# Optimization experiments

Hardware: AMD Instinct MI355X
Metric: run time of the kernel (lower is better)

## Reference

```python
import jax, jax.numpy as jnp
import numpy as np

L = 256  # grayscale_levels
THRESH = (50.0, 150.0)
BASE = (30, 80, 150)
INCR = (10, 15, 25)


def setup_inputs() -> dict:
    key = jax.random.key(0)
    image = jax.random.uniform(key, (8, 3, 1024, 1024), dtype=jnp.float32)
    return {"image": image}


def _glcm_contrast(gray_idx):
    # gray_idx: [H, W] int32 in [0, L). distance=1, angle=0 -> horizontal neighbor pairs.
    p1 = gray_idx[:, :-1].ravel()
    p2 = gray_idx[:, 1:].ravel()
    # 256x256 co-occurrence histogram via flattened scatter-add
    hist = jnp.zeros(L * L, jnp.float32).at[p1 * L + p2].add(1.0)
    hist = hist / jnp.float32(p1.size)
    lv = jnp.arange(L, dtype=jnp.float32)
    diff2 = (lv[:, None] - lv[None, :]) ** 2
    return jnp.sum(hist.reshape(L, L) * diff2)


def _grid_labels(H, W, n_segments):
    # Deterministic grid superpixels (stand-in for skimage SLIC's initial grid;
    # same downstream math: fill each segment with its region mean).
    gr = max(1, int(round(np.sqrt(n_segments * H / W))))
    gc = max(1, int(np.ceil(n_segments / gr)))
    r = (np.arange(H) * gr) // H
    c = (np.arange(W) * gc) // W
    labels = r[:, None] * gc + c[None, :]
    return jnp.asarray(labels, dtype=jnp.int32), gr * gc


def _region_mean_saliency(gray, labels, nseg):
    flat = labels.ravel()
    sums = jax.ops.segment_sum(gray.ravel(), flat, num_segments=nseg)
    cnts = jax.ops.segment_sum(jnp.ones_like(gray).ravel(), flat, num_segments=nseg)
    return (sums / jnp.maximum(cnts, 1.0))[labels]


def reference(image):
    B, C, H, W = image.shape
    gray = 0.299 * image[:, 0] + 0.587 * image[:, 1] + 0.114 * image[:, 2]
    gidx = jnp.clip((gray * (L - 1)).astype(jnp.int32), 0, L - 1)
    complexity = jax.vmap(_glcm_contrast)(gidx)  # [B]

    comp_np = np.asarray(jax.device_get(complexity))
    cluster_sets = []
    for cv in comp_np:
        tier = 0 if cv < THRESH[0] else (1 if cv < THRESH[1] else 2)
        k, d = BASE[tier], INCR[tier]
        cluster_sets.append([k - d, k, k + d])

    # region mean uses np.mean over all channels of the region -> channel-mean image
    chan_mean = image.mean(axis=1)  # [B, H, W]
    label_cache = {}
    sal_rows = []
    for i, cset in enumerate(cluster_sets):
        maps = []
        for n in cset:
            if n not in label_cache:
                label_cache[n] = _grid_labels(H, W, n)
            labels, nseg = label_cache[n]
            maps.append(_region_mean_saliency(chan_mean[i], labels, nseg))
        sal_rows.append(jnp.stack(maps))  # [3, H, W]
    saliency = jnp.stack(sal_rows)  # [B, 3, H, W]
    return saliency, complexity, jnp.asarray(cluster_sets, dtype=jnp.int32)
```

## Files before the change

### kernel.cpp

```cpp
#include <hip/hip_runtime.h>
#include <math.h>

#define HW 1024
#define PLANE (1024 * 1024)

typedef float vf4 __attribute__((ext_vector_type(4)));

__constant__ int GCS[8]   = {5, 6, 7, 9, 10, 12, 13, 14};
__constant__ int BBASE[8] = {0, 6, 13, 21, 31, 42, 55, 69};
__constant__ int GR9c[9]      = {4, 5, 6, 8, 9, 10, 11, 12, 13};
__constant__ int GC9c[9]      = {5, 6, 7, 9, 9, 10, 12, 13, 14};
__constant__ int COLBASE9c[9] = {0, 5, 11, 18, 18, 27, 37, 49, 62};


__device__ __forceinline__ int wave_reduce_int(int v) {
#pragma unroll
    for (int off = 32; off > 0; off >>= 1) v += __shfl_down(v, off, 64);
    return v;
}
__device__ __forceinline__ float wave_reduce_f(float v) {
#pragma unroll
    for (int off = 32; off > 0; off >>= 1) v += __shfl_down(v, off, 64);
    return v;
}

__device__ __forceinline__ unsigned short f2bf(float x) {
    unsigned int u = __float_as_uint(x);
    u += 0x7fff + ((u >> 16) & 1);
    return (unsigned short)(u >> 16);
}
__device__ __forceinline__ float bf2f(unsigned short s) {
    return __uint_as_float(((unsigned int)s) << 16);
}

__global__ __launch_bounds__(256) void k_main(const float* __restrict__ img,
                                              float* __restrict__ partials,
                                              float* __restrict__ rowrec) {
    const int b = blockIdx.y;
    const int tid = threadIdx.x;
    const int lane = tid & 63;
    const int w = tid >> 6;
    const int row = (blockIdx.x << 2) + w;

    const float* p = img + (size_t)b * (3 * PLANE) + row * HW;

    __shared__ unsigned short cmS[4][1024];
    __shared__ float PS[4][260];
    __shared__ float BS[4][88];
    __shared__ int swred[4];

    vf4 R[4], G[4], Bv[4];
#pragma unroll
    for (int j = 0; j < 4; ++j) {
        const int c = ((j << 6) + lane) << 2;
        R[j] = __builtin_nontemporal_load((const vf4*)(p + c));
        G[j] = __builtin_nontemporal_load((const vf4*)(p + PLANE + c));
        Bv[j] = __builtin_nontemporal_load((const vf4*)(p + 2 * PLANE + c));
    }

    int acc = 0;
    int pend = 0;
    float csum[4];

#pragma unroll
    for (int j = 0; j < 4; ++j) {
        const int c = ((j << 6) + lane) << 2;

        const float m0 = (R[j].x + G[j].x + Bv[j].x) * (1.0f / 3.0f);
        const float m1 = (R[j].y + G[j].y + Bv[j].y) * (1.0f / 3.0f);
        const float m2 = (R[j].z + G[j].z + Bv[j].z) * (1.0f / 3.0f);
        const float m3 = (R[j].w + G[j].w + Bv[j].w) * (1.0f / 3.0f);
        *(ushort4*)&cmS[w][c] = make_ushort4(f2bf(m0), f2bf(m1), f2bf(m2), f2bf(m3));
        csum[j] = (m0 + m1) + (m2 + m3);

        const float g0 = 0.299f * R[j].x + 0.587f * G[j].x + 0.114f * Bv[j].x;
        const float g1 = 0.299f * R[j].y + 0.587f * G[j].y + 0.114f * Bv[j].y;
        const float g2 = 0.299f * R[j].z + 0.587f * G[j].z + 0.114f * Bv[j].z;
        const float g3 = 0.299f * R[j].w + 0.587f * G[j].w + 0.114f * Bv[j].w;

        const int gi0 = min(max((int)(g0 * 255.0f), 0), 255);
        const int gi1 = min(max((int)(g1 * 255.0f), 0), 255);
        const int gi2 = min(max((int)(g2 * 255.0f), 0), 255);
        const int gi3 = min(max((int)(g3 * 255.0f), 0), 255);

        const int first0 = __shfl(gi0, 0, 64);
        if (j > 0 && lane == 63) {
            const int d = pend - first0;
            acc += d * d;
        }
        const int nxt = __shfl_down(gi0, 1, 64);
        const int d0 = gi0 - gi1, d1 = gi1 - gi2, d2 = gi2 - gi3;
        acc += d0 * d0 + d1 * d1 + d2 * d2;
        if (lane != 63) {
            const int d = gi3 - nxt;
            acc += d * d;
        }
        pend = gi3;
    }

    float pre = 0.0f;
#pragma unroll
    for (int j = 0; j < 4; ++j) {
        float x = csum[j];
#pragma unroll
        for (int off = 1; off < 64; off <<= 1) {
            const float y = __shfl_up(x, off, 64);
            if (lane >= off) x += y;
        }
        PS[w][(j << 6) + lane] = pre + (x - csum[j]);
        pre += __shfl(x, 63, 64);
    }
    if (lane == 0) PS[w][256] = pre;

#pragma unroll
    for (int rep = 0; rep < 2; ++rep) {
        const int bnd = lane + (rep << 6);
        if (bnd < 84) {
            const int sct = (bnd >= 6) + (bnd >= 13) + (bnd >= 21) + (bnd >= 31) +
                            (bnd >= 42) + (bnd >= 55) + (bnd >= 69);
            const int gc = GCS[sct];
            const int i = bnd - BBASE[sct];
            const int c = (i * 1024 + gc - 1) / gc;
            const int m = c & 3;
            const int cb = min(c & ~3, 1020);
            float Bp = PS[w][c >> 2];
            const float a0 = bf2f(cmS[w][cb]), a1 = bf2f(cmS[w][cb + 1]),
                        a2 = bf2f(cmS[w][cb + 2]);
            if (m > 0) Bp += a0;
            if (m > 1) Bp += a1;
            if (m > 2) Bp += a2;
            BS[w][bnd] = Bp;
        }
    }

    float* rr = rowrec + (size_t)((b << 10) + row) * 80;
#pragma unroll
    for (int rep = 0; rep < 2; ++rep) {
        const int k = lane + (rep << 6);
        if (k < 76) {
            const int sct = (k >= 5) + (k >= 11) + (k >= 18) + (k >= 27) +
                            (k >= 37) + (k >= 49) + (k >= 62);
            const int bidx = k + sct;
            rr[k] = BS[w][bidx + 1] - BS[w][bidx];
        }
    }

    acc = wave_reduce_int(acc);
    if (lane == 0) swred[w] = acc;
    __syncthreads();
    if (tid == 0)
        partials[(b << 8) + blockIdx.x] = (float)(swred[0] + swred[1] + swred[2] + swred[3]);
}

__global__ __launch_bounds__(256) void k_fill2(const float* __restrict__ partials,
                                               const float* __restrict__ rowrec,
                                               float* __restrict__ out) {
    const int rblk = blockIdx.x, jm = blockIdx.y, b = blockIdx.z;
    const int tid = threadIdx.x;
    const int lane = tid & 63, w = tid >> 6;

    __shared__ float compLDS[4];
    __shared__ int tierS;
    __shared__ float red[16][17];
    __shared__ float cmLDS[2][16];

    float v = partials[(b << 8) + tid];
    v = wave_reduce_f(v);
    if (lane == 0) compLDS[w] = v;
    __syncthreads();
    if (tid == 0) {
        const float cv = (compLDS[0] + compLDS[1] + compLDS[2] + compLDS[3]) *
                         (1.0f / (1024.0f * 1023.0f));
        const int tier = (cv < 50.0f) ? 0 : ((cv < 150.0f) ? 1 : 2);
        tierS = tier;
        if (rblk == 0 && jm == 0) {
            const size_t OFFC = (size_t)8 * 3 * PLANE;
            out[OFFC + b] = cv;
            const int kk = (tier == 0) ? 30 : ((tier == 1) ? 80 : 150);
            const int dd = (tier == 0) ? 10 : ((tier == 1) ? 15 : 25);
#pragma unroll
            for (int j = 0; j < 3; ++j)
                out[OFFC + 8 + b * 3 + j] = (float)(kk + (j - 1) * dd);
        }
    }
    __syncthreads();

    const int g = tierS * 3 + jm;
    const int gr = GR9c[g], gc = GC9c[g], cb = COLBASE9c[g];
    const int row0 = rblk << 2;
    const int rc0 = (row0 * gr) >> 10;
    const int rc3 = ((row0 + 3) * gr) >> 10;

    const int cc = tid & 15, rch = tid >> 4;
    for (int rc = rc0; rc <= rc3; ++rc) {
        const int r0 = (rc * 1024 + gr - 1) / gr;
        const int r1 = ((rc + 1) * 1024 + gr - 1) / gr;
        float s = 0.0f;
        if (cc < gc)
            for (int r = r0 + rch; r < r1; r += 16)
                s += rowrec[(size_t)((b << 10) + r) * 80 + cb + cc];
        red[rch][cc] = s;
        __syncthreads();
        if (rch == 0 && cc < gc) {
            float tot = 0.0f;
#pragma unroll
            for (int q = 0; q < 16; ++q) tot += red[q][cc];
            const int c0 = (cc * 1024 + gc - 1) / gc;
            const int c1 = ((cc + 1) * 1024 + gc - 1) / gc;
            const float area = (float)((r1 - r0) * (c1 - c0));
            cmLDS[rc - rc0][cc] = tot / area;
        }
        __syncthreads();
    }

    const int col = tid << 2;
    const int i0 = (col * gc) >> 10, i1 = ((col + 1) * gc) >> 10;
    const int i2 = ((col + 2) * gc) >> 10, i3 = ((col + 3) * gc) >> 10;
    float* ob = out + ((size_t)(b * 3 + jm) << 20);
#pragma unroll
    for (int i = 0; i < 4; ++i) {
        const int row = row0 + i;
        const int rc = (row * gr) >> 10;
        const float* cm = cmLDS[rc - rc0];
        vf4 o;
        o.x = cm[i0];
        o.y = cm[i1];
        o.z = cm[i2];
        o.w = cm[i3];
        __builtin_nontemporal_store(o, (vf4*)(ob + row * HW + col));
    }
}

extern "C" void kernel_launch(void* const* d_in, const int* in_sizes, int n_in,
                              void* d_out, int out_size, void* d_ws, size_t ws_size,
                              hipStream_t stream) {
    const float* img = (const float*)d_in[0];
    float* out = (float*)d_out;
    float* ws = (float*)d_ws;

    float* partials = ws;
    float* rowrec = ws + 16384;

    k_main<<<dim3(256, 8), 256, 0, stream>>>(img, partials, rowrec);
    k_fill2<<<dim3(256, 3, 8), 256, 0, stream>>>(partials, rowrec, out);
}
```

Before: 45.10 us.

## Process four rows per wave with register double-buffered prefetch in k_main

Each block now handles 16 rows instead of 4, with every wave looping over four rows. The next row's RGB vectors are loaded into a second register set while the current row is processed, so global load latency overlaps compute. The grid shrinks from 256x8 to 64x8 blocks and the partials layout in k_fill2 is adjusted to match. This raises register pressure and leaves only 512 blocks on a large GPU, which can lower occupancy and memory-level parallelism.

New measurement: 47.46 us. 1.05x slower.

```diff
diff --git a/kernel.cpp b/kernel.cpp
--- a/kernel.cpp
+++ b/kernel.cpp
@@ -37,111 +37,141 @@
                                               float* __restrict__ partials,
                                               float* __restrict__ rowrec) {
     const int b = blockIdx.y;
+    const int rb = blockIdx.x;
     const int tid = threadIdx.x;
     const int lane = tid & 63;
     const int w = tid >> 6;
-    const int row = (blockIdx.x << 2) + w;
-
-    const float* p = img + (size_t)b * (3 * PLANE) + row * HW;
+
+    const float* pb = img + (size_t)b * (3 * PLANE);
 
     __shared__ unsigned short cmS[4][1024];
     __shared__ float PS[4][260];
     __shared__ float BS[4][88];
     __shared__ int swred[4];
 
-    vf4 R[4], G[4], Bv[4];
-#pragma unroll
-    for (int j = 0; j < 4; ++j) {
-        const int c = ((j << 6) + lane) << 2;
-        R[j] = __builtin_nontemporal_load((const vf4*)(p + c));
-        G[j] = __builtin_nontemporal_load((const vf4*)(p + PLANE + c));
-        Bv[j] = __builtin_nontemporal_load((const vf4*)(p + 2 * PLANE + c));
+    const int coff[4] = {(lane << 2), ((64 + lane) << 2), ((128 + lane) << 2),
+                         ((192 + lane) << 2)};
+
+    vf4 RA[4], GA[4], BA[4], RN[4], GN[4], BN[4];
+    {
+        const float* p = pb + ((rb << 4) + w) * HW;
+#pragma unroll
+        for (int j = 0; j < 4; ++j) {
+            RA[j] = __builtin_nontemporal_load((const vf4*)(p + coff[j]));
+            GA[j] = __builtin_nontemporal_load((const vf4*)(p + PLANE + coff[j]));
+            BA[j] = __builtin_nontemporal_load((const vf4*)(p + 2 * PLANE + coff[j]));
+        }
     }
 
     int acc = 0;
-    int pend = 0;
-    float csum[4];
-
-#pragma unroll
-    for (int j = 0; j < 4; ++j) {
-        const int c = ((j << 6) + lane) << 2;
-
-        const float m0 = (R[j].x + G[j].x + Bv[j].x) * (1.0f / 3.0f);
-        const float m1 = (R[j].y + G[j].y + Bv[j].y) * (1.0f / 3.0f);
-        const float m2 = (R[j].z + G[j].z + Bv[j].z) * (1.0f / 3.0f);
-        const float m3 = (R[j].w + G[j].w + Bv[j].w) * (1.0f / 3.0f);
-        *(ushort4*)&cmS[w][c] = make_ushort4(f2bf(m0), f2bf(m1), f2bf(m2), f2bf(m3));
-        csum[j] = (m0 + m1) + (m2 + m3);
-
-        const float g0 = 0.299f * R[j].x + 0.587f * G[j].x + 0.114f * Bv[j].x;
-        const float g1 = 0.299f * R[j].y + 0.587f * G[j].y + 0.114f * Bv[j].y;
-        const float g2 = 0.299f * R[j].z + 0.587f * G[j].z + 0.114f * Bv[j].z;
-        const float g3 = 0.299f * R[j].w + 0.587f * G[j].w + 0.114f * Bv[j].w;
-
-        const int gi0 = min(max((int)(g0 * 255.0f), 0), 255);
-        const int gi1 = min(max((int)(g1 * 255.0f), 0), 255);
-        const int gi2 = min(max((int)(g2 * 255.0f), 0), 255);
-        const int gi3 = min(max((int)(g3 * 255.0f), 0), 255);
-
-        const int first0 = __shfl(gi0, 0, 64);
-        if (j > 0 && lane == 63) {
-            const int d = pend - first0;
-            acc += d * d;
-        }
-        const int nxt = __shfl_down(gi0, 1, 64);
-        const int d0 = gi0 - gi1, d1 = gi1 - gi2, d2 = gi2 - gi3;
-        acc += d0 * d0 + d1 * d1 + d2 * d2;
-        if (lane != 63) {
-            const int d = gi3 - nxt;
-            acc += d * d;
-        }
-        pend = gi3;
-    }
-
-    float pre = 0.0f;
-#pragma unroll
-    for (int j = 0; j < 4; ++j) {
-        float x = csum[j];
-#pragma unroll
-        for (int off = 1; off < 64; off <<= 1) {
-            const float y = __shfl_up(x, off, 64);
-            if (lane >= off) x += y;
-        }
-        PS[w][(j << 6) + lane] = pre + (x - csum[j]);
-        pre += __shfl(x, 63, 64);
-    }
-    if (lane == 0) PS[w][256] = pre;
-
-#pragma unroll
-    for (int rep = 0; rep < 2; ++rep) {
-        const int bnd = lane + (rep << 6);
-        if (bnd < 84) {
-            const int sct = (bnd >= 6) + (bnd >= 13) + (bnd >= 21) + (bnd >= 31) +
-                            (bnd >= 42) + (bnd >= 55) + (bnd >= 69);
-            const int gc = GCS[sct];
-            const int i = bnd - BBASE[sct];
-            const int c = (i * 1024 + gc - 1) / gc;
-            const int m = c & 3;
-            const int cb = min(c & ~3, 1020);
-            float Bp = PS[w][c >> 2];
-            const float a0 = bf2f(cmS[w][cb]), a1 = bf2f(cmS[w][cb + 1]),
-                        a2 = bf2f(cmS[w][cb + 2]);
-            if (m > 0) Bp += a0;
-            if (m > 1) Bp += a1;
-            if (m > 2) Bp += a2;
-            BS[w][bnd] = Bp;
-        }
-    }
-
-    float* rr = rowrec + (size_t)((b << 10) + row) * 80;
-#pragma unroll
-    for (int rep = 0; rep < 2; ++rep) {
-        const int k = lane + (rep << 6);
-        if (k < 76) {
-            const int sct = (k >= 5) + (k >= 11) + (k >= 18) + (k >= 27) +
-                            (k >= 37) + (k >= 49) + (k >= 62);
-            const int bidx = k + sct;
-            rr[k] = BS[w][bidx + 1] - BS[w][bidx];
+
+#pragma unroll
+    for (int it = 0; it < 4; ++it) {
+        const int row = (rb << 4) + (it << 2) + w;
+
+        if (it < 3) {
+            const float* pn = pb + (row + 4) * HW;
+#pragma unroll
+            for (int j = 0; j < 4; ++j) {
+                RN[j] = __builtin_nontemporal_load((const vf4*)(pn + coff[j]));
+                GN[j] = __builtin_nontemporal_load((const vf4*)(pn + PLANE + coff[j]));
+                BN[j] = __builtin_nontemporal_load((const vf4*)(pn + 2 * PLANE + coff[j]));
+            }
+        }
+
+        int pend = 0;
+        float csum[4];
+
+#pragma unroll
+        for (int j = 0; j < 4; ++j) {
+            const int c = coff[j];
+
+            const float m0 = (RA[j].x + GA[j].x + BA[j].x) * (1.0f / 3.0f);
+            const float m1 = (RA[j].y + GA[j].y + BA[j].y) * (1.0f / 3.0f);
+            const float m2 = (RA[j].z + GA[j].z + BA[j].z) * (1.0f / 3.0f);
+            const float m3 = (RA[j].w + GA[j].w + BA[j].w) * (1.0f / 3.0f);
+            *(ushort4*)&cmS[w][c] = make_ushort4(f2bf(m0), f2bf(m1), f2bf(m2), f2bf(m3));
+            csum[j] = (m0 + m1) + (m2 + m3);
+
+            const float g0 = 0.299f * RA[j].x + 0.587f * GA[j].x + 0.114f * BA[j].x;
+            const float g1 = 0.299f * RA[j].y + 0.587f * GA[j].y + 0.114f * BA[j].y;
+            const float g2 = 0.299f * RA[j].z + 0.587f * GA[j].z + 0.114f * BA[j].z;
+            const float g3 = 0.299f * RA[j].w + 0.587f * GA[j].w + 0.114f * BA[j].w;
+
+            const int gi0 = min(max((int)(g0 * 255.0f), 0), 255);
+            const int gi1 = min(max((int)(g1 * 255.0f), 0), 255);
+            const int gi2 = min(max((int)(g2 * 255.0f), 0), 255);
+            const int gi3 = min(max((int)(g3 * 255.0f), 0), 255);
+
+            const int first0 = __shfl(gi0, 0, 64);
+            if (j > 0 && lane == 63) {
+                const int d = pend - first0;
+                acc += d * d;
+            }
+            const int nxt = __shfl_down(gi0, 1, 64);
+            const int d0 = gi0 - gi1, d1 = gi1 - gi2, d2 = gi2 - gi3;
+            acc += d0 * d0 + d1 * d1 + d2 * d2;
+            if (lane != 63) {
+                const int d = gi3 - nxt;
+                acc += d * d;
+            }
+            pend = gi3;
+        }
+
+        float pre = 0.0f;
+#pragma unroll
+        for (int j = 0; j < 4; ++j) {
+            float x = csum[j];
+#pragma unroll
+            for (int off = 1; off < 64; off <<= 1) {
+                const float y = __shfl_up(x, off, 64);
+                if (lane >= off) x += y;
+            }
+            PS[w][(j << 6) + lane] = pre + (x - csum[j]);
+            pre += __shfl(x, 63, 64);
+        }
+        if (lane == 0) PS[w][256] = pre;
+
+#pragma unroll
+        for (int rep = 0; rep < 2; ++rep) {
+            const int bnd = lane + (rep << 6);
+            if (bnd < 84) {
+                const int sct = (bnd >= 6) + (bnd >= 13) + (bnd >= 21) + (bnd >= 31) +
+                                (bnd >= 42) + (bnd >= 55) + (bnd >= 69);
+                const int gc = GCS[sct];
+                const int i = bnd - BBASE[sct];
+                const int c = (i * 1024 + gc - 1) / gc;
+                const int m = c & 3;
+                const int cb = min(c & ~3, 1020);
+                float Bp = PS[w][c >> 2];
+                const float a0 = bf2f(cmS[w][cb]), a1 = bf2f(cmS[w][cb + 1]),
+                            a2 = bf2f(cmS[w][cb + 2]);
+                if (m > 0) Bp += a0;
+                if (m > 1) Bp += a1;
+                if (m > 2) Bp += a2;
+                BS[w][bnd] = Bp;
+            }
+        }
+
+        float* rr = rowrec + (size_t)((b << 10) + row) * 80;
+#pragma unroll
+        for (int rep = 0; rep < 2; ++rep) {
+            const int k = lane + (rep << 6);
+            if (k < 76) {
+                const int sct = (k >= 5) + (k >= 11) + (k >= 18) + (k >= 27) +
+                                (k >= 37) + (k >= 49) + (k >= 62);
+                const int bidx = k + sct;
+                rr[k] = BS[w][bidx + 1] - BS[w][bidx];
+            }
+        }
+
+        if (it < 3) {
+#pragma unroll
+            for (int j = 0; j < 4; ++j) {
+                RA[j] = RN[j];
+                GA[j] = GN[j];
+                BA[j] = BN[j];
+            }
         }
     }
 
@@ -149,7 +179,7 @@
     if (lane == 0) swred[w] = acc;
     __syncthreads();
     if (tid == 0)
-        partials[(b << 8) + blockIdx.x] = (float)(swred[0] + swred[1] + swred[2] + swred[3]);
+        partials[(b << 6) + rb] = (float)(swred[0] + swred[1] + swred[2] + swred[3]);
 }
 
 __global__ __launch_bounds__(256) void k_fill2(const float* __restrict__ partials,
@@ -164,7 +194,7 @@
     __shared__ float red[16][17];
     __shared__ float cmLDS[2][16];
 
-    float v = partials[(b << 8) + tid];
+    float v = (tid < 64) ? partials[(b << 6) + tid] : 0.0f;
     v = wave_reduce_f(v);
     if (lane == 0) compLDS[w] = v;
     __syncthreads();
@@ -241,6 +271,6 @@
     float* partials = ws;
     float* rowrec = ws + 16384;
 
-    k_main<<<dim3(256, 8), 256, 0, stream>>>(img, partials, rowrec);
+    k_main<<<dim3(64, 8), 256, 0, stream>>>(img, partials, rowrec);
     k_fill2<<<dim3(256, 3, 8), 256, 0, stream>>>(partials, rowrec, out);
 }
```
